# Kernel optimization log

Hardware: AMD Instinct MI355X
Metric: run time of the kernel (lower is better)

The kernel has to match this reference:

```python
import jax, jax.numpy as jnp
import numpy as np

D_MODEL, D_FFN, N_EXPERTS, TOP_K = 1024, 4096, 8, 2
BATCH, SEQ = 4, 1024


def setup_inputs() -> dict:
    key = jax.random.key(0)
    kx, kr, k1, k2, k3 = jax.random.split(key, 5)
    scale = 0.02
    return {
        "x": jax.random.normal(kx, (BATCH, SEQ, D_MODEL), dtype=jnp.float32),
        "w_router": jax.random.normal(kr, (D_MODEL, N_EXPERTS), dtype=jnp.float32) * scale,
        "w1": jax.random.normal(k1, (N_EXPERTS, D_MODEL, D_FFN), dtype=jnp.float32) * scale,
        "w2": jax.random.normal(k2, (N_EXPERTS, D_FFN, D_MODEL), dtype=jnp.float32) * scale,
        "w3": jax.random.normal(k3, (N_EXPERTS, D_MODEL, D_FFN), dtype=jnp.float32) * scale,
    }


def reference(x, w_router, w1, w2, w3):
    B, S, D = x.shape
    E = w_router.shape[1]
    T = B * S
    xf = x.reshape(T, D)

    # --- router: softmax over experts, top-k, renormalize ---
    router_probs = jax.nn.softmax(xf @ w_router, axis=-1)          # (T, E)
    topk_probs, topk_idx = jax.lax.top_k(router_probs, TOP_K)      # (T, K)
    topk_probs = topk_probs / topk_probs.sum(axis=-1, keepdims=True)

    # per-token combine weight for each expert (top_k indices are distinct,
    # matching the torch per-slot accumulation exactly)
    comb = jnp.zeros((T, E), dtype=xf.dtype)
    comb = comb.at[jnp.arange(T)[:, None], topk_idx].add(topk_probs)  # (T, E)

    # --- dense SwiGLU experts (same math as masked loop) ---
    h = jnp.einsum("td,edf->tef", xf, w1)                          # (T, E, F)
    g = jnp.einsum("td,edf->tef", xf, w3)                          # (T, E, F)
    y = jnp.einsum("tef,efd->ted", jax.nn.silu(h) * g, w2)         # (T, E, D)
    out = jnp.einsum("te,ted->td", comb, y).reshape(B, S, D)

    # --- load-balance aux loss ---
    expert_mask = jax.nn.one_hot(topk_idx, E, dtype=jnp.float32).sum(axis=1)  # (T, E)
    tokens_per_expert = expert_mask.sum(axis=0) / T
    mean_probs = router_probs.mean(axis=0)
    aux_loss = E * jnp.sum(tokens_per_expert * mean_probs)
    return out, aux_loss
```

## Files before the change

### kernel.cpp

```cpp
#include <hip/hip_runtime.h>
#include <hip/hip_bf16.h>
#include <cstdint>
#include <cstddef>

#define TT 4096
#define DM 1024
#define DF 4096
#define NE 8
#define BTAB 72
#define BTAB2 40

typedef __attribute__((ext_vector_type(8))) short bf16x8;
typedef __attribute__((ext_vector_type(8))) unsigned short ushort8;
typedef __attribute__((ext_vector_type(4))) float f32x4;

static __device__ __forceinline__ unsigned short f2bf(float f) {
    union { float f; unsigned int u; } v; v.f = f;
    unsigned int u = v.u;
    return (unsigned short)((u + 0x7FFFu + ((u >> 16) & 1u)) >> 16);
}
static __device__ __forceinline__ float bf2f(unsigned short h) {
    union { unsigned int u; float f; } v; v.u = ((unsigned int)h) << 16;
    return v.f;
}

#define GLOAD16(gsrc, ldst)                                                        \
    __builtin_amdgcn_global_load_lds(                                              \
        (const __attribute__((address_space(1))) void*)(gsrc),                     \
        (__attribute__((address_space(3))) void*)(ldst), 16, 0, 0)

__global__ void transpose_v2(const float* __restrict__ in,
                             unsigned short* __restrict__ out,
                             int R, int C) {
    __shared__ float tile[64][65];
    const int e = blockIdx.z;
    const float* src = in + (size_t)e * R * C;
    unsigned short* dst = out + (size_t)e * R * C;
    const int c0 = blockIdx.x * 64, r0 = blockIdx.y * 64;
    const int tid = threadIdx.x;
    #pragma unroll
    for (int i = 0; i < 4; ++i) {
        int idx = tid + i * 256;
        int rr = idx >> 4, cc = idx & 15;
        float4 v = *(const float4*)(src + (size_t)(r0 + rr) * C + c0 + cc * 4);
        tile[rr][cc * 4 + 0] = v.x;
        tile[rr][cc * 4 + 1] = v.y;
        tile[rr][cc * 4 + 2] = v.z;
        tile[rr][cc * 4 + 3] = v.w;
    }
    __syncthreads();
    #pragma unroll
    for (int i = 0; i < 2; ++i) {
        int idx = tid + i * 256;
        int c = idx >> 3, rc = idx & 7;
        ushort8 o;
        #pragma unroll
        for (int j = 0; j < 8; ++j) o[j] = f2bf(tile[rc * 8 + j][c]);
        *(ushort8*)(dst + (size_t)(c0 + c) * R + r0 + rc * 8) = o;
    }
}

__global__ void router_kernel(const float* __restrict__ x,
                              const float* __restrict__ wr,
                              unsigned short* __restrict__ xb,
                              int* __restrict__ topi, float* __restrict__ topw,
                              float* __restrict__ probsum) {
    __shared__ float s_ps[NE];
    const int tid = threadIdx.x;
    if (tid < NE) s_ps[tid] = 0.f;
    __syncthreads();
    const int wid = tid >> 6, lane = tid & 63;
    const int t = blockIdx.x * 4 + wid;
    float acc[NE] = {0.f, 0.f, 0.f, 0.f, 0.f, 0.f, 0.f, 0.f};
    const float* xr = x + (size_t)t * DM;
    unsigned short* xbr = xb + (size_t)t * DM;
    for (int it = 0; it < DM / 64; ++it) {
        int d = it * 64 + lane;
        float xv = xr[d];
        xbr[d] = f2bf(xv);
        const float* w = wr + d * NE;
        #pragma unroll
        for (int e = 0; e < NE; ++e) acc[e] = fmaf(xv, w[e], acc[e]);
    }
    #pragma unroll
    for (int e = 0; e < NE; ++e) {
        float v = acc[e];
        #pragma unroll
        for (int off = 32; off; off >>= 1) v += __shfl_xor(v, off);
        acc[e] = v;
    }
    if (lane == 0) {
        float m = acc[0];
        #pragma unroll
        for (int e = 1; e < NE; ++e) m = fmaxf(m, acc[e]);
        float p[NE], s = 0.f;
        #pragma unroll
        for (int e = 0; e < NE; ++e) { p[e] = expf(acc[e] - m); s += p[e]; }
        float inv = 1.f / s;
        #pragma unroll
        for (int e = 0; e < NE; ++e) { p[e] *= inv; atomicAdd(&s_ps[e], p[e]); }
        int i1 = 0; float p1 = p[0];
        #pragma unroll
        for (int e = 1; e < NE; ++e) if (p[e] > p1) { p1 = p[e]; i1 = e; }
        int i2 = -1; float p2 = -1.f;
        #pragma unroll
        for (int e = 0; e < NE; ++e) if (e != i1 && p[e] > p2) { p2 = p[e]; i2 = e; }
        float rs = 1.f / (p1 + p2);
        topi[t * 2] = i1; topi[t * 2 + 1] = i2;
        topw[t * 2] = p1 * rs; topw[t * 2 + 1] = p2 * rs;
    }
    __syncthreads();
    if (tid < NE) atomicAdd(&probsum[tid], s_ps[tid]);
}

__global__ void assign_kernel(const int* __restrict__ topi,
                              int* __restrict__ list, int* __restrict__ slotpos,
                              int* __restrict__ cnt) {
    const int e = blockIdx.x;
    __shared__ int s_wc[4];
    const int tid = threadIdx.x, wid = tid >> 6, lane = tid & 63;
    int running = 0;
    for (int base = 0; base < TT; base += 256) {
        int t = base + tid;
        int hit = 0, slot = 0;
        int a = topi[2 * t], b = topi[2 * t + 1];
        if (a == e) { hit = 1; slot = 0; }
        else if (b == e) { hit = 1; slot = 1; }
        unsigned long long m = __ballot(hit);
        if (lane == 0) s_wc[wid] = __popcll(m);
        __syncthreads();
        int pre = 0, tot = 0;
        #pragma unroll
        for (int q = 0; q < 4; ++q) { int c = s_wc[q]; tot += c; if (q < wid) pre += c; }
        if (hit) {
            int pos = running + pre + __popcll(m & ((1ull << lane) - 1ull));
            list[e * TT + pos] = t;
            slotpos[2 * t + slot] = pos;
        }
        running += tot;
        __syncthreads();
    }
    if (tid == 0) cnt[e] = running;
}

__global__ void finalize_kernel(const int* __restrict__ cnt,
                                const float* __restrict__ probsum,
                                int* __restrict__ offs,
                                unsigned int* __restrict__ blocktab,
                                unsigned int* __restrict__ blocktab2,
                                float* __restrict__ out_aux) {
    int o = 0;
    float aux = 0.f;
    int nb = 0, nb2 = 0;
    for (int e = 0; e < NE; ++e) {
        offs[e] = o; o += cnt[e];
        aux += (float)cnt[e] * probsum[e];
        int nrb = (cnt[e] + 127) >> 7;
        for (int rb = 0; rb < nrb; ++rb) blocktab[nb++] = ((unsigned)e << 16) | rb;
        int nrb2 = (cnt[e] + 255) >> 8;
        for (int rb = 0; rb < nrb2; ++rb) blocktab2[nb2++] = ((unsigned)e << 16) | rb;
    }
    while (nb < BTAB) blocktab[nb++] = 0xFFFFFFFFu;
    while (nb2 < BTAB2) blocktab2[nb2++] = 0xFFFFFFFFu;
    *out_aux = (float)NE * aux / ((float)TT * (float)TT);
}

__global__ __launch_bounds__(512, 1) void gemm1_kernel(
    const unsigned short* __restrict__ xb,
    const unsigned short* __restrict__ w1T,
    const unsigned short* __restrict__ w3T,
    unsigned short* __restrict__ act,
    const int* __restrict__ list,
    const int* __restrict__ cnt,
    const int* __restrict__ offs,
    const unsigned int* __restrict__ blocktab2) {
    const int lin = blockIdx.y * 32 + blockIdx.x;
    const int xcd = lin & 7, j = lin >> 3;
    const int fcolb = xcd * 4 + (j & 3);
    const int slot = j >> 2;
    const unsigned int tab = blocktab2[slot];
    if (tab == 0xFFFFFFFFu) return;
    const int e = tab >> 16;
    const int rowbase = (int)(tab & 0xFFFFu) << 8;
    const int ce = cnt[e];
    const int fbase = fcolb * 128;

    __shared__ __align__(16) unsigned short lds[65536];
    char* ldsC = (char*)lds;

    const int tid = threadIdx.x;
    const int lane = tid & 63, wid = tid >> 6;
    const int wm = wid >> 2, wn = wid & 3;

    const unsigned short* aP[2][2];
    const unsigned short* bP[2][2];
    #pragma unroll
    for (int ci = 0; ci < 2; ++ci) {
        const int c = tid + ci * 512;
        const int r = (c >> 2) & 15, rg = c >> 7, cc = c & 3, ks = (c >> 6) & 1;
        const int row = rg * 16 + r;
        const int kb = ks * 64 + ((cc * 16) ^ ((r & 8) << 2));
        #pragma unroll
        for (int h = 0; h < 2; ++h) {
            int sp = rowbase + h * 128 + row; if (sp >= ce) sp = ce - 1;
            aP[h][ci] = xb + (size_t)list[e * TT + sp] * DM + (kb >> 1);
            const int n = h * 128 + row;
            const int col = fbase + (n >> 5) * 16 + (n & 15);
            const unsigned short* wsrc = ((n >> 4) & 1) ? w3T : w1T;
            bP[h][ci] = wsrc + ((size_t)e * DF + col) * DM + (kb >> 1);
        }
    }

#define STG_A(H, T, B) {                                                          \
    GLOAD16(aP[H][0] + (size_t)(T) * 64, ldsC + (B) * 65536 + (H) * 16384 + tid * 16);        \
    GLOAD16(aP[H][1] + (size_t)(T) * 64, ldsC + (B) * 65536 + (H) * 16384 + 8192 + tid * 16); }
#define STG_B(H, T, B) {                                                          \
    GLOAD16(bP[H][0] + (size_t)(T) * 64, ldsC + (B) * 65536 + 32768 + (H) * 16384 + tid * 16);        \
    GLOAD16(bP[H][1] + (size_t)(T) * 64, ldsC + (B) * 65536 + 32768 + (H) * 16384 + 8192 + tid * 16); }

    const int lofs = ((lane & 15) << 6) + ((((lane >> 4) << 4) ^ ((lane & 8) << 2)));

#define RDA(BB, MQ) { _Pragma("unroll") for (int i = 0; i < 4; ++i) {             \
    _Pragma("unroll") for (int k2 = 0; k2 < 2; ++k2)                              \
        aq[i][k2] = *(const bf16x8*)(ldsC + (BB) + wm * 16384 +                   \
                     (((MQ) * 4 + i) * 2 + k2) * 1024 + lofs); } }
#define RDB(DST, BB, NQ) { _Pragma("unroll") for (int u = 0; u < 2; ++u) {        \
    _Pragma("unroll") for (int k2 = 0; k2 < 2; ++k2)                              \
        DST[u][k2] = *(const bf16x8*)(ldsC + (BB) + 32768 + (wn >> 1) * 16384 +   \
                     (wn & 1) * 8192 + ((NQ) * 2 + u) * 2048 + k2 * 1024 + lofs); } }
#define MMQ(MQ, NQ, BQ) { __builtin_amdgcn_s_setprio(1);                          \
    _Pragma("unroll") for (int i = 0; i < 4; ++i)                                 \
    _Pragma("unroll") for (int u = 0; u < 2; ++u)                                 \
    _Pragma("unroll") for (int k2 = 0; k2 < 2; ++k2)                              \
        acc[(MQ) * 4 + i][(NQ) * 2 + u] = __builtin_amdgcn_mfma_f32_16x16x32_bf16(\
            aq[i][k2], BQ[u][k2], acc[(MQ) * 4 + i][(NQ) * 2 + u], 0, 0, 0);      \
    __builtin_amdgcn_s_setprio(0); }

    f32x4 acc[8][4] = {};
    bf16x8 aq[4][2], b0[2][2], b1[2][2];

    STG_A(0, 0, 0); STG_A(1, 0, 0); STG_B(0, 0, 0); STG_B(1, 0, 0);
    STG_B(0, 1, 1); STG_B(1, 1, 1); STG_A(0, 1, 1);
    asm volatile("s_waitcnt vmcnt(6)" ::: "memory");
    __builtin_amdgcn_s_barrier();

    #pragma unroll 1
    for (int h = 0; h < 16; ++h) {
        const int bb = (h & 1) * 65536;
        RDA(bb, 0) RDB(b0, bb, 0)
        if (h < 15) STG_A(1, h + 1, (h & 1) ^ 1);
        MMQ(0, 0, b0)
        __builtin_amdgcn_s_barrier();
        RDB(b1, bb, 1)
        MMQ(0, 1, b1)
        __builtin_amdgcn_s_barrier();
        RDA(bb, 1)
        if (h < 14) STG_B(0, h + 2, h & 1);
        MMQ(1, 0, b0)
        __builtin_amdgcn_s_barrier();
        if (h < 14) { STG_B(1, h + 2, h & 1); STG_A(0, h + 2, h & 1); }
        MMQ(1, 1, b1)
        if (h < 14)       { asm volatile("s_waitcnt vmcnt(6)" ::: "memory"); }
        else if (h == 14) { asm volatile("s_waitcnt vmcnt(0)" ::: "memory"); }
        __builtin_amdgcn_s_barrier();
    }
#undef STG_A
#undef STG_B
#undef RDA
#undef RDB
#undef MMQ

    const int ob = offs[e];
    const int g = lane >> 4, rr = lane & 15;
    #pragma unroll
    for (int m = 0; m < 8; ++m) {
        #pragma unroll
        for (int j2 = 0; j2 < 4; ++j2) {
            const int pos = rowbase + wm * 128 + m * 16 + g * 4 + j2;
            if (pos < ce) {
                unsigned short* arow = act + (size_t)(ob + pos) * DF + fbase + wn * 32;
                #pragma unroll
                for (int p = 0; p < 2; ++p) {
                    float hv = acc[m][2 * p][j2];
                    float gv = acc[m][2 * p + 1][j2];
                    float a = (hv / (1.f + __expf(-hv))) * gv;
                    arow[p * 16 + rr] = f2bf(a);
                }
            }
        }
    }
}

__global__ __launch_bounds__(256, 2) void gemm2_kernel(
    const unsigned short* __restrict__ act,
    const unsigned short* __restrict__ w2T,
    unsigned short* __restrict__ ybuf,
    const int* __restrict__ cnt,
    const int* __restrict__ offs,
    const unsigned int* __restrict__ blocktab) {
    const unsigned int tab = blocktab[blockIdx.y];
    if (tab == 0xFFFFFFFFu) return;
    const int e = tab >> 16;
    const int rowbase = (int)(tab & 0xFFFFu) << 7;
    const int ce = cnt[e];
    const int ob = offs[e];
    const int dbase = blockIdx.x * 128;

    __shared__ __align__(16) unsigned short lds[32768];
    char* ldsC = (char*)lds;

    const int tid = threadIdx.x;
    const int lane = tid & 63, wid = tid >> 6;
    const int wm = wid >> 1, wn = wid & 1;

    const unsigned short* aP[4];
    const unsigned short* bP[4];
    #pragma unroll
    for (int ci = 0; ci < 4; ++ci) {
        const int c = tid + ci * 256;
        const int rg = c >> 7, ks = (c >> 6) & 1, r = (c >> 2) & 15, cc = c & 3;
        const int row = rg * 16 + r;
        const int kb = ks * 64 + ((cc * 16) ^ ((r & 8) << 2));
        int sp = rowbase + row; if (sp >= ce) sp = ce - 1;
        aP[ci] = act + (size_t)(ob + sp) * DF + (kb >> 1);
        bP[ci] = w2T + ((size_t)e * DM + dbase + row) * DF + (kb >> 1);
    }

#define STG2(T, B) { _Pragma("unroll") for (int ci = 0; ci < 4; ++ci) {           \
        GLOAD16(aP[ci] + (size_t)(T) * 64, ldsC + (B) * 32768 + ci * 4096 + tid * 16);         \
        GLOAD16(bP[ci] + (size_t)(T) * 64, ldsC + (B) * 32768 + 16384 + ci * 4096 + tid * 16); } }

    const int lofs = ((lane & 15) << 6) + ((((lane >> 4) << 4) ^ ((lane & 8) << 2)));

    f32x4 acc[4][4] = {};

    const int NT = DF / 64;
    STG2(0, 0)
    asm volatile("s_waitcnt vmcnt(0)" ::: "memory");
    __builtin_amdgcn_s_barrier();

    #pragma unroll 2
    for (int h = 0; h < NT; ++h) {
        const int bb = (h & 1) * 32768;
        if (h + 1 < NT) STG2(h + 1, (h & 1) ^ 1)
        bf16x8 aq[4][2], bq[4][2];
        #pragma unroll
        for (int m = 0; m < 4; ++m)
            #pragma unroll
            for (int k2 = 0; k2 < 2; ++k2)
                aq[m][k2] = *(const bf16x8*)(ldsC + bb + (wm * 4 + m) * 2048 + k2 * 1024 + lofs);
        #pragma unroll
        for (int u = 0; u < 4; ++u)
            #pragma unroll
            for (int k2 = 0; k2 < 2; ++k2)
                bq[u][k2] = *(const bf16x8*)(ldsC + bb + 16384 + (wn * 4 + u) * 2048 + k2 * 1024 + lofs);
        __builtin_amdgcn_sched_barrier(0);
        __builtin_amdgcn_s_setprio(1);
        #pragma unroll
        for (int k2 = 0; k2 < 2; ++k2)
            #pragma unroll
            for (int u = 0; u < 4; ++u)
                #pragma unroll
                for (int m = 0; m < 4; ++m)
                    acc[m][u] = __builtin_amdgcn_mfma_f32_16x16x32_bf16(aq[m][k2], bq[u][k2], acc[m][u], 0, 0, 0);
        __builtin_amdgcn_s_setprio(0);
        if (h + 1 < NT) {
            asm volatile("s_waitcnt vmcnt(0)" ::: "memory");
            __builtin_amdgcn_s_barrier();
        }
    }
#undef STG2

    const int g = lane >> 4, rr = lane & 15;
    #pragma unroll
    for (int m = 0; m < 4; ++m) {
        #pragma unroll
        for (int j2 = 0; j2 < 4; ++j2) {
            const int pos = rowbase + wm * 64 + m * 16 + g * 4 + j2;
            if (pos < ce) {
                unsigned short* yrow = ybuf + (size_t)(ob + pos) * DM + dbase + wn * 64;
                #pragma unroll
                for (int u = 0; u < 4; ++u)
                    yrow[u * 16 + rr] = f2bf(acc[m][u][j2]);
            }
        }
    }
}

__global__ void combine_kernel(const unsigned short* __restrict__ ybuf,
                               const int* __restrict__ topi,
                               const float* __restrict__ topw,
                               const int* __restrict__ slotpos,
                               const int* __restrict__ offs,
                               float* __restrict__ out) {
    const int t = blockIdx.x;
    const int tid = threadIdx.x;
    const int e0 = topi[2 * t], e1 = topi[2 * t + 1];
    const int r0 = offs[e0] + slotpos[2 * t];
    const int r1 = offs[e1] + slotpos[2 * t + 1];
    const float w0 = topw[2 * t], w1 = topw[2 * t + 1];
    ushort4 a = *(const ushort4*)(ybuf + (size_t)r0 * DM + tid * 4);
    ushort4 b = *(const ushort4*)(ybuf + (size_t)r1 * DM + tid * 4);
    float4 o;
    o.x = w0 * bf2f(a.x) + w1 * bf2f(b.x);
    o.y = w0 * bf2f(a.y) + w1 * bf2f(b.y);
    o.z = w0 * bf2f(a.z) + w1 * bf2f(b.z);
    o.w = w0 * bf2f(a.w) + w1 * bf2f(b.w);
    *(float4*)(out + (size_t)t * DM + tid * 4) = o;
}

extern "C" void kernel_launch(void* const* d_in, const int* in_sizes, int n_in,
                              void* d_out, int out_size, void* d_ws, size_t ws_size,
                              hipStream_t stream) {
    (void)in_sizes; (void)n_in; (void)ws_size;
    const float* x  = (const float*)d_in[0];
    const float* wr = (const float*)d_in[1];
    const float* w1 = (const float*)d_in[2];
    const float* w2 = (const float*)d_in[3];
    const float* w3 = (const float*)d_in[4];
    float* out = (float*)d_out;

    char* ws = (char*)d_ws;
    size_t off = 0;
    auto alloc = [&](size_t bytes) -> void* {
        void* p = ws + off;
        off = (off + bytes + 255) & ~(size_t)255;
        return p;
    };
    unsigned short* w1T = (unsigned short*)alloc((size_t)NE * DF * DM * 2);
    unsigned short* w3T = (unsigned short*)alloc((size_t)NE * DF * DM * 2);
    unsigned short* w2T = (unsigned short*)alloc((size_t)NE * DM * DF * 2);
    unsigned short* act = (unsigned short*)alloc((size_t)2 * TT * DF * 2);
    unsigned short* xb  = (unsigned short*)alloc((size_t)TT * DM * 2);
    int*   topi    = (int*)alloc(TT * 2 * sizeof(int));
    float* topw    = (float*)alloc(TT * 2 * sizeof(float));
    int*   list    = (int*)alloc((size_t)NE * TT * sizeof(int));
    int*   slotpos = (int*)alloc(TT * 2 * sizeof(int));
    int*   cnt     = (int*)alloc(NE * sizeof(int));
    int*   offs    = (int*)alloc(NE * sizeof(int));
    float* probsum = (float*)alloc(NE * sizeof(float));
    unsigned int* blocktab  = (unsigned int*)alloc(BTAB * sizeof(unsigned int));
    unsigned int* blocktab2 = (unsigned int*)alloc(BTAB2 * sizeof(unsigned int));
    unsigned short* ybuf = w1T;

    hipMemsetAsync(probsum, 0, NE * sizeof(float), stream);

    dim3 tb(256);
    transpose_v2<<<dim3(DF / 64, DM / 64, NE), tb, 0, stream>>>(w1, w1T, DM, DF);
    transpose_v2<<<dim3(DF / 64, DM / 64, NE), tb, 0, stream>>>(w3, w3T, DM, DF);
    transpose_v2<<<dim3(DM / 64, DF / 64, NE), tb, 0, stream>>>(w2, w2T, DF, DM);

    router_kernel<<<TT / 4, 256, 0, stream>>>(x, wr, xb, topi, topw, probsum);
    assign_kernel<<<NE, 256, 0, stream>>>(topi, list, slotpos, cnt);
    finalize_kernel<<<1, 1, 0, stream>>>(cnt, probsum, offs, blocktab, blocktab2, out + (out_size - 1));

    gemm1_kernel<<<dim3(32, BTAB2), 512, 0, stream>>>(xb, w1T, w3T, act, list, cnt, offs, blocktab2);
    gemm2_kernel<<<dim3(8, BTAB), 256, 0, stream>>>(act, w2T, ybuf, cnt, offs, blocktab);
    combine_kernel<<<TT, 256, 0, stream>>>(ybuf, topi, topw, slotpos, offs, out);
}
```

Baseline: 432.3 us.

## Make gemm2 a persistent kernel with atomic tile queue

```diff
diff --git a/kernel.cpp b/kernel.cpp
--- a/kernel.cpp
+++ b/kernel.cpp
@@ -148,6 +148,7 @@
                                 int* __restrict__ offs,
                                 unsigned int* __restrict__ blocktab,
                                 unsigned int* __restrict__ blocktab2,
+                                int* __restrict__ work,
                                 float* __restrict__ out_aux) {
     int o = 0;
     float aux = 0.f;
@@ -160,6 +161,7 @@
         int nrb2 = (cnt[e] + 255) >> 8;
         for (int rb = 0; rb < nrb2; ++rb) blocktab2[nb2++] = ((unsigned)e << 16) | rb;
     }
+    work[1] = nb * 8;
     while (nb < BTAB) blocktab[nb++] = 0xFFFFFFFFu;
     while (nb2 < BTAB2) blocktab2[nb2++] = 0xFFFFFFFFu;
     *out_aux = (float)NE * aux / ((float)TT * (float)TT);
@@ -297,93 +299,106 @@
     unsigned short* __restrict__ ybuf,
     const int* __restrict__ cnt,
     const int* __restrict__ offs,
-    const unsigned int* __restrict__ blocktab) {
-    const unsigned int tab = blocktab[blockIdx.y];
-    if (tab == 0xFFFFFFFFu) return;
-    const int e = tab >> 16;
-    const int rowbase = (int)(tab & 0xFFFFu) << 7;
-    const int ce = cnt[e];
-    const int ob = offs[e];
-    const int dbase = blockIdx.x * 128;
-
+    const unsigned int* __restrict__ blocktab,
+    int* __restrict__ work) {
     __shared__ __align__(16) unsigned short lds[32768];
+    __shared__ int s_t;
     char* ldsC = (char*)lds;
 
     const int tid = threadIdx.x;
     const int lane = tid & 63, wid = tid >> 6;
     const int wm = wid >> 1, wn = wid & 1;
-
-    const unsigned short* aP[4];
-    const unsigned short* bP[4];
+    const int lofs = ((lane & 15) << 6) + ((((lane >> 4) << 4) ^ ((lane & 8) << 2)));
+    const int ntiles = work[1];
+
+    int srow[4], skb[4];
     #pragma unroll
     for (int ci = 0; ci < 4; ++ci) {
         const int c = tid + ci * 256;
         const int rg = c >> 7, ks = (c >> 6) & 1, r = (c >> 2) & 15, cc = c & 3;
-        const int row = rg * 16 + r;
-        const int kb = ks * 64 + ((cc * 16) ^ ((r & 8) << 2));
-        int sp = rowbase + row; if (sp >= ce) sp = ce - 1;
-        aP[ci] = act + (size_t)(ob + sp) * DF + (kb >> 1);
-        bP[ci] = w2T + ((size_t)e * DM + dbase + row) * DF + (kb >> 1);
-    }
+        srow[ci] = rg * 16 + r;
+        skb[ci] = ks * 64 + ((cc * 16) ^ ((r & 8) << 2));
+    }
+
+    for (;;) {
+        if (tid == 0) s_t = atomicAdd(&work[0], 1);
+        __syncthreads();
+        const int t = s_t;
+        if (t >= ntiles) return;
+        const unsigned int tab = blocktab[t >> 3];
+        const int e = tab >> 16;
+        const int rowbase = (int)(tab & 0xFFFFu) << 7;
+        const int ce = cnt[e];
+        const int ob = offs[e];
+        const int dbase = (t & 7) * 128;
+
+        const unsigned short* aP[4];
+        const unsigned short* bP[4];
+        #pragma unroll
+        for (int ci = 0; ci < 4; ++ci) {
+            int sp = rowbase + srow[ci]; if (sp >= ce) sp = ce - 1;
+            aP[ci] = act + (size_t)(ob + sp) * DF + (skb[ci] >> 1);
+            bP[ci] = w2T + ((size_t)e * DM + dbase + srow[ci]) * DF + (skb[ci] >> 1);
+        }
 
 #define STG2(T, B) { _Pragma("unroll") for (int ci = 0; ci < 4; ++ci) {           \
         GLOAD16(aP[ci] + (size_t)(T) * 64, ldsC + (B) * 32768 + ci * 4096 + tid * 16);         \
         GLOAD16(bP[ci] + (size_t)(T) * 64, ldsC + (B) * 32768 + 16384 + ci * 4096 + tid * 16); } }
 
-    const int lofs = ((lane & 15) << 6) + ((((lane >> 4) << 4) ^ ((lane & 8) << 2)));
-
-    f32x4 acc[4][4] = {};
-
-    const int NT = DF / 64;
-    STG2(0, 0)
-    asm volatile("s_waitcnt vmcnt(0)" ::: "memory");
-    __builtin_amdgcn_s_barrier();
-
-    #pragma unroll 2
-    for (int h = 0; h < NT; ++h) {
-        const int bb = (h & 1) * 32768;
-        if (h + 1 < NT) STG2(h + 1, (h & 1) ^ 1)
-        bf16x8 aq[4][2], bq[4][2];
-        #pragma unroll
-        for (int m = 0; m < 4; ++m)
+        f32x4 acc[4][4] = {};
+
+        const int NT = DF / 64;
+        STG2(0, 0)
+        asm volatile("s_waitcnt vmcnt(0)" ::: "memory");
+        __builtin_amdgcn_s_barrier();
+
+        #pragma unroll 2
+        for (int h = 0; h < NT; ++h) {
+            const int bb = (h & 1) * 32768;
+            if (h + 1 < NT) STG2(h + 1, (h & 1) ^ 1)
+            bf16x8 aq[4][2], bq[4][2];
             #pragma unroll
-            for (int k2 = 0; k2 < 2; ++k2)
-                aq[m][k2] = *(const bf16x8*)(ldsC + bb + (wm * 4 + m) * 2048 + k2 * 1024 + lofs);
-        #pragma unroll
-        for (int u = 0; u < 4; ++u)
-            #pragma unroll
-            for (int k2 = 0; k2 < 2; ++k2)
-                bq[u][k2] = *(const bf16x8*)(ldsC + bb + 16384 + (wn * 4 + u) * 2048 + k2 * 1024 + lofs);
-        __builtin_amdgcn_sched_barrier(0);
-        __builtin_amdgcn_s_setprio(1);
-        #pragma unroll
-        for (int k2 = 0; k2 < 2; ++k2)
+            for (int m = 0; m < 4; ++m)
+                #pragma unroll
+                for (int k2 = 0; k2 < 2; ++k2)
+                    aq[m][k2] = *(const bf16x8*)(ldsC + bb + (wm * 4 + m) * 2048 + k2 * 1024 + lofs);
             #pragma unroll
             for (int u = 0; u < 4; ++u)
                 #pragma unroll
-                for (int m = 0; m < 4; ++m)
-                    acc[m][u] = __builtin_amdgcn_mfma_f32_16x16x32_bf16(aq[m][k2], bq[u][k2], acc[m][u], 0, 0, 0);
-        __builtin_amdgcn_s_setprio(0);
-        if (h + 1 < NT) {
-            asm volatile("s_waitcnt vmcnt(0)" ::: "memory");
-            __builtin_amdgcn_s_barrier();
-        }
-    }
-#undef STG2
-
-    const int g = lane >> 4, rr = lane & 15;
-    #pragma unroll
-    for (int m = 0; m < 4; ++m) {
-        #pragma unroll
-        for (int j2 = 0; j2 < 4; ++j2) {
-            const int pos = rowbase + wm * 64 + m * 16 + g * 4 + j2;
-            if (pos < ce) {
-                unsigned short* yrow = ybuf + (size_t)(ob + pos) * DM + dbase + wn * 64;
+                for (int k2 = 0; k2 < 2; ++k2)
+                    bq[u][k2] = *(const bf16x8*)(ldsC + bb + 16384 + (wn * 4 + u) * 2048 + k2 * 1024 + lofs);
+            __builtin_amdgcn_sched_barrier(0);
+            __builtin_amdgcn_s_setprio(1);
+            #pragma unroll
+            for (int k2 = 0; k2 < 2; ++k2)
                 #pragma unroll
                 for (int u = 0; u < 4; ++u)
-                    yrow[u * 16 + rr] = f2bf(acc[m][u][j2]);
+                    #pragma unroll
+                    for (int m = 0; m < 4; ++m)
+                        acc[m][u] = __builtin_amdgcn_mfma_f32_16x16x32_bf16(aq[m][k2], bq[u][k2], acc[m][u], 0, 0, 0);
+            __builtin_amdgcn_s_setprio(0);
+            if (h + 1 < NT) {
+                asm volatile("s_waitcnt vmcnt(0)" ::: "memory");
+                __builtin_amdgcn_s_barrier();
             }
         }
+#undef STG2
+
+        const int g = lane >> 4, rr = lane & 15;
+        #pragma unroll
+        for (int m = 0; m < 4; ++m) {
+            #pragma unroll
+            for (int j2 = 0; j2 < 4; ++j2) {
+                const int pos = rowbase + wm * 64 + m * 16 + g * 4 + j2;
+                if (pos < ce) {
+                    unsigned short* yrow = ybuf + (size_t)(ob + pos) * DM + dbase + wn * 64;
+                    #pragma unroll
+                    for (int u = 0; u < 4; ++u)
+                        yrow[u * 16 + rr] = f2bf(acc[m][u][j2]);
+                }
+            }
+        }
+        __syncthreads();
     }
 }
 
@@ -441,9 +456,11 @@
     float* probsum = (float*)alloc(NE * sizeof(float));
     unsigned int* blocktab  = (unsigned int*)alloc(BTAB * sizeof(unsigned int));
     unsigned int* blocktab2 = (unsigned int*)alloc(BTAB2 * sizeof(unsigned int));
+    int* work = (int*)alloc(2 * sizeof(int));
     unsigned short* ybuf = w1T;
 
     hipMemsetAsync(probsum, 0, NE * sizeof(float), stream);
+    hipMemsetAsync(work, 0, 2 * sizeof(int), stream);
 
     dim3 tb(256);
     transpose_v2<<<dim3(DF / 64, DM / 64, NE), tb, 0, stream>>>(w1, w1T, DM, DF);
@@ -452,9 +469,9 @@
 
     router_kernel<<<TT / 4, 256, 0, stream>>>(x, wr, xb, topi, topw, probsum);
     assign_kernel<<<NE, 256, 0, stream>>>(topi, list, slotpos, cnt);
-    finalize_kernel<<<1, 1, 0, stream>>>(cnt, probsum, offs, blocktab, blocktab2, out + (out_size - 1));
+    finalize_kernel<<<1, 1, 0, stream>>>(cnt, probsum, offs, blocktab, blocktab2, work, out + (out_size - 1));
 
     gemm1_kernel<<<dim3(32, BTAB2), 512, 0, stream>>>(xb, w1T, w3T, act, list, cnt, offs, blocktab2);
-    gemm2_kernel<<<dim3(8, BTAB), 256, 0, stream>>>(act, w2T, ybuf, cnt, offs, blocktab);
+    gemm2_kernel<<<512, 256, 0, stream>>>(act, w2T, ybuf, cnt, offs, blocktab, work);
     combine_kernel<<<TT, 256, 0, stream>>>(ybuf, topi, topw, slotpos, offs, out);
 }
```

Measured after the change: 446.3 us. +3.2%, slower.

## Fuse weight transposes and router into one launch; trim gemm1 barriers

Applied to the files above, without the earlier changes.

```diff
diff --git a/kernel.cpp b/kernel.cpp
--- a/kernel.cpp
+++ b/kernel.cpp
@@ -29,48 +29,54 @@
         (const __attribute__((address_space(1))) void*)(gsrc),                     \
         (__attribute__((address_space(3))) void*)(ldst), 16, 0, 0)
 
-__global__ void transpose_v2(const float* __restrict__ in,
-                             unsigned short* __restrict__ out,
-                             int R, int C) {
+__global__ void prep_kernel(const float* __restrict__ w1, const float* __restrict__ w3,
+                            const float* __restrict__ w2,
+                            unsigned short* __restrict__ w1T, unsigned short* __restrict__ w3T,
+                            unsigned short* __restrict__ w2T,
+                            const float* __restrict__ x, const float* __restrict__ wr,
+                            unsigned short* __restrict__ xb,
+                            int* __restrict__ topi, float* __restrict__ topw,
+                            float* __restrict__ probsum) {
     __shared__ float tile[64][65];
-    const int e = blockIdx.z;
-    const float* src = in + (size_t)e * R * C;
-    unsigned short* dst = out + (size_t)e * R * C;
-    const int c0 = blockIdx.x * 64, r0 = blockIdx.y * 64;
+    const int b = blockIdx.x;
     const int tid = threadIdx.x;
-    #pragma unroll
-    for (int i = 0; i < 4; ++i) {
-        int idx = tid + i * 256;
-        int rr = idx >> 4, cc = idx & 15;
-        float4 v = *(const float4*)(src + (size_t)(r0 + rr) * C + c0 + cc * 4);
-        tile[rr][cc * 4 + 0] = v.x;
-        tile[rr][cc * 4 + 1] = v.y;
-        tile[rr][cc * 4 + 2] = v.z;
-        tile[rr][cc * 4 + 3] = v.w;
-    }
-    __syncthreads();
-    #pragma unroll
-    for (int i = 0; i < 2; ++i) {
-        int idx = tid + i * 256;
-        int c = idx >> 3, rc = idx & 7;
-        ushort8 o;
-        #pragma unroll
-        for (int j = 0; j < 8; ++j) o[j] = f2bf(tile[rc * 8 + j][c]);
-        *(ushort8*)(dst + (size_t)(c0 + c) * R + r0 + rc * 8) = o;
-    }
-}
-
-__global__ void router_kernel(const float* __restrict__ x,
-                              const float* __restrict__ wr,
-                              unsigned short* __restrict__ xb,
-                              int* __restrict__ topi, float* __restrict__ topw,
-                              float* __restrict__ probsum) {
-    __shared__ float s_ps[NE];
-    const int tid = threadIdx.x;
+    if (b < 24576) {
+        const float* in; unsigned short* out; int R, C, cx, ry;
+        const int bb = b & 8191;
+        const int e = bb >> 10;
+        if (b < 8192)       { in = w1; out = w1T; R = DM; C = DF; cx = bb & 63; ry = (bb >> 6) & 15; }
+        else if (b < 16384) { in = w3; out = w3T; R = DM; C = DF; cx = bb & 63; ry = (bb >> 6) & 15; }
+        else                { in = w2; out = w2T; R = DF; C = DM; cx = bb & 15; ry = (bb >> 4) & 63; }
+        const float* src = in + (size_t)e * R * C;
+        unsigned short* dst = out + (size_t)e * R * C;
+        const int c0 = cx * 64, r0 = ry * 64;
+        #pragma unroll
+        for (int i = 0; i < 4; ++i) {
+            int idx = tid + i * 256;
+            int rr = idx >> 4, cc = idx & 15;
+            float4 v = *(const float4*)(src + (size_t)(r0 + rr) * C + c0 + cc * 4);
+            tile[rr][cc * 4 + 0] = v.x;
+            tile[rr][cc * 4 + 1] = v.y;
+            tile[rr][cc * 4 + 2] = v.z;
+            tile[rr][cc * 4 + 3] = v.w;
+        }
+        __syncthreads();
+        #pragma unroll
+        for (int i = 0; i < 2; ++i) {
+            int idx = tid + i * 256;
+            int c = idx >> 3, rc = idx & 7;
+            ushort8 o;
+            #pragma unroll
+            for (int j = 0; j < 8; ++j) o[j] = f2bf(tile[rc * 8 + j][c]);
+            *(ushort8*)(dst + (size_t)(c0 + c) * R + r0 + rc * 8) = o;
+        }
+        return;
+    }
+    float* s_ps = &tile[0][0];
     if (tid < NE) s_ps[tid] = 0.f;
     __syncthreads();
     const int wid = tid >> 6, lane = tid & 63;
-    const int t = blockIdx.x * 4 + wid;
+    const int t = (b - 24576) * 4 + wid;
     float acc[NE] = {0.f, 0.f, 0.f, 0.f, 0.f, 0.f, 0.f, 0.f};
     const float* xr = x + (size_t)t * DM;
     unsigned short* xbr = xb + (size_t)t * DM;
@@ -250,15 +256,12 @@
         RDA(bb, 0) RDB(b0, bb, 0)
         if (h < 15) STG_A(1, h + 1, (h & 1) ^ 1);
         MMQ(0, 0, b0)
-        __builtin_amdgcn_s_barrier();
         RDB(b1, bb, 1)
         MMQ(0, 1, b1)
-        __builtin_amdgcn_s_barrier();
         RDA(bb, 1)
-        if (h < 14) STG_B(0, h + 2, h & 1);
         MMQ(1, 0, b0)
         __builtin_amdgcn_s_barrier();
-        if (h < 14) { STG_B(1, h + 2, h & 1); STG_A(0, h + 2, h & 1); }
+        if (h < 14) { STG_B(0, h + 2, h & 1); STG_B(1, h + 2, h & 1); STG_A(0, h + 2, h & 1); }
         MMQ(1, 1, b1)
         if (h < 14)       { asm volatile("s_waitcnt vmcnt(6)" ::: "memory"); }
         else if (h == 14) { asm volatile("s_waitcnt vmcnt(0)" ::: "memory"); }
@@ -445,12 +448,8 @@
 
     hipMemsetAsync(probsum, 0, NE * sizeof(float), stream);
 
-    dim3 tb(256);
-    transpose_v2<<<dim3(DF / 64, DM / 64, NE), tb, 0, stream>>>(w1, w1T, DM, DF);
-    transpose_v2<<<dim3(DF / 64, DM / 64, NE), tb, 0, stream>>>(w3, w3T, DM, DF);
-    transpose_v2<<<dim3(DM / 64, DF / 64, NE), tb, 0, stream>>>(w2, w2T, DF, DM);
-
-    router_kernel<<<TT / 4, 256, 0, stream>>>(x, wr, xb, topi, topw, probsum);
+    prep_kernel<<<25600, 256, 0, stream>>>(w1, w3, w2, w1T, w3T, w2T,
+                                           x, wr, xb, topi, topw, probsum);
     assign_kernel<<<NE, 256, 0, stream>>>(topi, list, slotpos, cnt);
     finalize_kernel<<<1, 1, 0, stream>>>(cnt, probsum, offs, blocktab, blocktab2, out + (out_size - 1));
 
```

Result: faster. 422.7 us, median of 4 (-2.2%).
